# Optimization experiments

Hardware: AMD Instinct MI355X
Metric: run time of the kernel (lower is better)

## Reference

```python
import jax, jax.numpy as jnp
import numpy as np

B, S, H = 2, 2048, 2048
NH, NKV, HD = 16, 4, 128
THETA = 10000.0


def _rope_cos_sin(seq_len, head_dim, theta, dtype):
    inv_freq = 1.0 / (theta ** (jnp.arange(0, head_dim, 2, dtype=jnp.float32) / head_dim))
    t = jnp.arange(seq_len, dtype=jnp.float32)
    freqs = t[:, None] * inv_freq[None, :]          # [S, HD/2]
    emb = jnp.concatenate([freqs, freqs], axis=-1)  # [S, HD]
    return jnp.cos(emb).astype(dtype), jnp.sin(emb).astype(dtype)


def _rotate_half(x):
    d = x.shape[-1] // 2
    return jnp.concatenate([-x[..., d:], x[..., :d]], axis=-1)


def setup_inputs() -> dict:
    key = jax.random.key(0)
    ks = jax.random.split(key, 5)
    x = jax.random.normal(ks[0], (B, S, H), dtype=jnp.float32)
    Wq = jax.random.normal(ks[1], (NH * HD, H), dtype=jnp.float32) * 0.02
    Wk = jax.random.normal(ks[2], (NKV * HD, H), dtype=jnp.float32) * 0.02
    Wv = jax.random.normal(ks[3], (NKV * HD, H), dtype=jnp.float32) * 0.02
    Wo = jax.random.normal(ks[4], (H, H), dtype=jnp.float32) * 0.02
    causal = jnp.tril(jnp.ones((S, S), dtype=bool))
    attention_mask = jnp.where(causal, 0.0, -1e9).astype(jnp.float32)[None, None]  # [1,1,S,S]
    return {"x": x, "attention_mask": attention_mask, "Wq": Wq, "Wk": Wk, "Wv": Wv, "Wo": Wo}


def reference(x, attention_mask, Wq, Wk, Wv, Wo):
    b, s, _ = x.shape
    q = (x @ Wq.T).reshape(b, s, NH, HD).transpose(0, 2, 1, 3)    # [b,nh,s,hd]
    k = (x @ Wk.T).reshape(b, s, NKV, HD).transpose(0, 2, 1, 3)   # [b,nkv,s,hd]
    v = (x @ Wv.T).reshape(b, s, NKV, HD).transpose(0, 2, 1, 3)
    cos, sin = _rope_cos_sin(s, HD, THETA, x.dtype)               # [s,hd] each
    cos = cos[None, None]; sin = sin[None, None]
    q = q * cos + _rotate_half(q) * sin
    k = k * cos + _rotate_half(k) * sin
    rep = NH // NKV
    k = jnp.repeat(k, rep, axis=1)                                 # [b,nh,s,hd]
    v = jnp.repeat(v, rep, axis=1)
    scores = jnp.einsum('bhqd,bhkd->bhqk', q, k) / jnp.sqrt(jnp.asarray(HD, x.dtype))
    scores = scores + attention_mask
    attn = jax.nn.softmax(scores, axis=-1)
    out = jnp.einsum('bhqk,bhkd->bhqd', attn, v)                   # [b,nh,s,hd]
    out = out.transpose(0, 2, 1, 3).reshape(b, s, NH * HD)
    return out @ Wo.T
```

## Files before the change

kernel.cpp:

```cpp
#include <hip/hip_runtime.h>

typedef unsigned short u16;
typedef __bf16 bf16x8 __attribute__((ext_vector_type(8)));
typedef float f32x4 __attribute__((ext_vector_type(4)));
typedef short s16x4 __attribute__((ext_vector_type(4)));

#define S_LEN  2048
#define NHEADS 16
#define NKVH   4
#define HDIM   128
#define BB     2
#define MROWS  4096
#define QKV_N  3072
#define HID    2048

__device__ __forceinline__ u16 f2b(float f) {
  union { float f; unsigned u; } x; x.f = f;
  unsigned r = x.u + 0x7fffu + ((x.u >> 16) & 1u);
  return (u16)(r >> 16);
}
__device__ __forceinline__ float b2f(u16 v) {
  union { unsigned u; float f; } x; x.u = ((unsigned)v) << 16;
  return x.f;
}
__device__ __forceinline__ void gload_lds16(const u16* g, u16* l) {
  __builtin_amdgcn_global_load_lds((__attribute__((address_space(1))) void*)g,
                                   (__attribute__((address_space(3))) void*)l,
                                   16, 0, 0);
}
__device__ __forceinline__ unsigned cvtpk(float lo, float hi) {
  unsigned r;
  asm("v_cvt_pk_bf16_f32 %0, %1, %2" : "=v"(r) : "v"(lo), "v"(hi));
  return r;
}
#if __has_builtin(__builtin_amdgcn_mfma_f32_16x16x16bf16_1k)
__device__ __forceinline__ f32x4 mfma16(s16x4 a, s16x4 b, f32x4 c) {
  return __builtin_amdgcn_mfma_f32_16x16x16bf16_1k(a, b, c, 0, 0, 0);
}
#else
__device__ __forceinline__ f32x4 mfma16(s16x4 a, s16x4 b, f32x4 c) {
  f32x4 d;
  asm volatile("v_mfma_f32_16x16x16_bf16 %0, %1, %2, %3"
               : "=v"(d) : "v"(a), "v"(b), "v"(c));
  return d;
}
#endif

#define PB_X   8192
#define PB_WQ  (PB_X + 4096)
#define PB_WK  (PB_WQ + 1024)
#define PB_WV  (PB_WK + 1024)
#define PB_WO  (PB_WV + 4096)
#define PB_CS  (PB_WO + 512)
__global__ void k_prep(const float* __restrict__ x,
                       const float* __restrict__ Wq, const float* __restrict__ Wk,
                       const float* __restrict__ Wv, const float* __restrict__ Wo,
                       u16* __restrict__ xb, u16* __restrict__ Wqkvb,
                       u16* __restrict__ Wob, float* __restrict__ cs)
{
  const int bid = blockIdx.x, tid = threadIdx.x;
  const float* src; u16* dst; int i;
  if (bid < PB_X)       { i = bid * 256 + tid;            src = x;  dst = xb; }
  else if (bid < PB_WQ) { i = (bid - PB_X) * 256 + tid;   src = Wq; dst = Wqkvb; }
  else if (bid < PB_WK) { i = (bid - PB_WQ) * 256 + tid;  src = Wk; dst = Wqkvb + (size_t)2048 * HID; }
  else if (bid < PB_WV) { i = (bid - PB_WK) * 256 + tid;  src = Wv; dst = Wqkvb + (size_t)2560 * HID; }
  else if (bid < PB_WO) { i = (bid - PB_WV) * 256 + tid;  src = Wo; dst = Wob; }
  else {
    const int p = (bid - PB_WO) * 256 + tid;
    const int s = p >> 6, j = p & 63;
    float inv = expf(-(float)j * 0.14391156831212787f);
    float ang = (float)s * inv;
    float c, sn; sincosf(ang, &sn, &c);
    cs[p * 2 + 0] = c; cs[p * 2 + 1] = sn;
    return;
  }
  float4 v = ((const float4*)src)[i];
  ushort4 o;
  o.x = f2b(v.x); o.y = f2b(v.y); o.z = f2b(v.z); o.w = f2b(v.w);
  ((ushort4*)dst)[i] = o;
}

template <int OUT_BF16>
__global__ __launch_bounds__(256) void k_gemm_bt(
    const u16* __restrict__ A, const u16* __restrict__ Bm, void* __restrict__ Cv,
    int M, int N, int K)
{
  __shared__ u16 Al[128 * 32];
  __shared__ u16 Bl[128 * 32];
  const int tid = threadIdx.x;
  const int wave = tid >> 6, lane = tid & 63;
  const int l15 = lane & 15, l4 = lane >> 4;
  const int wr = wave >> 1, wc = wave & 1;
  const int row0 = blockIdx.y * 128, col0 = blockIdx.x * 128;

  f32x4 zero = {0.f, 0.f, 0.f, 0.f};
  f32x4 acc[4][4];
#pragma unroll
  for (int m = 0; m < 4; ++m)
#pragma unroll
    for (int n = 0; n < 4; ++n) acc[m][n] = zero;

  const int e0 = lane * 8;
  for (int kb = 0; kb < K; kb += 32) {
#pragma unroll
    for (int it = 0; it < 2; ++it) {
      const int chunk = it * 4 + wave;
      const int e = chunk * 512 + e0;
      const int r = e >> 5, c = e & 31;
      gload_lds16(A + (size_t)(row0 + r) * K + kb + c, Al + chunk * 512);
      gload_lds16(Bm + (size_t)(col0 + r) * K + kb + c, Bl + chunk * 512);
    }
    __syncthreads();
    bf16x8 af[4], bfv[4];
#pragma unroll
    for (int m = 0; m < 4; ++m)
      af[m] = *(const bf16x8*)(Al + (wr * 64 + m * 16 + l15) * 32 + l4 * 8);
#pragma unroll
    for (int n = 0; n < 4; ++n)
      bfv[n] = *(const bf16x8*)(Bl + (wc * 64 + n * 16 + l15) * 32 + l4 * 8);
#pragma unroll
    for (int m = 0; m < 4; ++m)
#pragma unroll
      for (int n = 0; n < 4; ++n)
        acc[m][n] = __builtin_amdgcn_mfma_f32_16x16x32_bf16(af[m], bfv[n], acc[m][n], 0, 0, 0);
    __syncthreads();
  }
#pragma unroll
  for (int m = 0; m < 4; ++m) {
    const int r = row0 + wr * 64 + m * 16 + l4 * 4;
#pragma unroll
    for (int n = 0; n < 4; ++n) {
      const int c = col0 + wc * 64 + n * 16 + l15;
#pragma unroll
      for (int j = 0; j < 4; ++j) {
        const float v = acc[m][n][j];
        if (OUT_BF16) ((u16*)Cv)[(size_t)(r + j) * N + c] = f2b(v);
        else          ((float*)Cv)[(size_t)(r + j) * N + c] = v;
      }
    }
  }
}

__global__ __launch_bounds__(256) void k_ropev(
    const u16* __restrict__ qkv, const float* __restrict__ cs,
    u16* __restrict__ Qr, u16* __restrict__ Kr, u16* __restrict__ Vt)
{
  const int blk = blockIdx.x;
  const int b = blk >> 8, s0 = (blk & 255) << 3;
  const int tid = threadIdx.x;
  const float S2 = 0.08838834764831845f * 1.4426950408889634f;
#pragma unroll
  for (int p = tid; p < 8192; p += 256) {
    const int s = p >> 10, rem = p & 1023, h = rem >> 6, j = rem & 63;
    const int sg = s0 + s;
    const float c = cs[(sg * 64 + j) * 2], sn = cs[(sg * 64 + j) * 2 + 1];
    const u16* src = qkv + (size_t)(b * S_LEN + sg) * QKV_N + h * 128;
    const float x0 = b2f(src[j]), x1 = b2f(src[64 + j]);
    const size_t base = ((size_t)(b * NHEADS + h) * S_LEN + sg) * HDIM;
    Qr[base + j]      = f2b((x0 * c - x1 * sn) * S2);
    Qr[base + 64 + j] = f2b((x1 * c + x0 * sn) * S2);
  }
#pragma unroll
  for (int p = tid; p < 2048; p += 256) {
    const int s = p >> 8, rem = p & 255, h = rem >> 6, j = rem & 63;
    const int sg = s0 + s;
    const float c = cs[(sg * 64 + j) * 2], sn = cs[(sg * 64 + j) * 2 + 1];
    const u16* src = qkv + (size_t)(b * S_LEN + sg) * QKV_N + 2048 + h * 128;
    const float x0 = b2f(src[j]), x1 = b2f(src[64 + j]);
    const size_t base = ((size_t)(b * NKVH + h) * S_LEN + sg) * HDIM;
    Kr[base + j]      = f2b(x0 * c - x1 * sn);
    Kr[base + 64 + j] = f2b(x1 * c + x0 * sn);
  }
#pragma unroll
  for (int vi = 0; vi < 2; ++vi) {
    const int idx = vi * 256 + tid, h = idx >> 7, d = idx & 127;
    union { u16 u[8]; uint4 v; } bb;
#pragma unroll
    for (int s = 0; s < 8; ++s)
      bb.u[s] = qkv[(size_t)(b * S_LEN + s0 + s) * QKV_N + 2560 + idx];
    *(uint4*)(Vt + ((size_t)(b * NKVH + h) * HDIM + d) * S_LEN + s0) = bb.v;
  }
}

__device__ __forceinline__ void attn_qtile(
    int qt, int lastPhase,
    const u16* __restrict__ Q, const u16* __restrict__ Kg, const u16* __restrict__ Vg,
    u16* __restrict__ Out, int bh,
    u16* Kl0, u16* Kl1, u16* Vl0, u16* Vl1,
    const int (&ko)[4], const int (&vo)[4],
    int wave, int lane, int& cur)
{
  const int l15 = lane & 15, l4 = lane >> 4;
  const int b = bh >> 4, h = bh & 15;
  const int qw0 = qt * 64 + wave * 16;
  const u16* Qg = Q + ((size_t)bh * S_LEN + qw0) * HDIM;

  bf16x8 qf[4];
#pragma unroll
  for (int kc = 0; kc < 4; ++kc)
    qf[kc] = *(const bf16x8*)(Qg + l15 * HDIM + kc * 32 + l4 * 8);

  f32x4 zero = {0.f, 0.f, 0.f, 0.f};
  f32x4 oacc[8];
#pragma unroll
  for (int i = 0; i < 8; ++i) oacc[i] = zero;
  float m_r = -1e30f, l_p = 0.f;

  const int nt = qt + 1;
  const int qg = qw0 + l15;

  for (int t = 0; t < nt; ++t) {
    const int kt = t * 64;
    u16* Vb = cur ? Vl1 : Vl0;
#pragma unroll
    for (int it = 0; it < 4; ++it)
      gload_lds16(Vg + (size_t)vo[it] + kt, Vb + (it * 4 + wave) * 512);
    const int hasNext = (t + 1 < nt) || (!lastPhase);
    const int ktn = (t + 1 < nt) ? kt + 64 : 0;
    u16* Kn = cur ? Kl0 : Kl1;
    if (hasNext) {
#pragma unroll
      for (int it = 0; it < 4; ++it)
        gload_lds16(Kg + (size_t)ktn * HDIM + ko[it], Kn + (it * 4 + wave) * 512);
      asm volatile("s_waitcnt vmcnt(8)" ::: "memory");
    } else {
      asm volatile("s_waitcnt vmcnt(4)" ::: "memory");
    }
    __builtin_amdgcn_sched_barrier(0);
    __builtin_amdgcn_s_barrier();
    __builtin_amdgcn_sched_barrier(0);

    const char* Kb = (const char*)(cur ? Kl1 : Kl0);
    f32x4 s[4];
#pragma unroll
    for (int n = 0; n < 4; ++n) s[n] = zero;
    __builtin_amdgcn_s_setprio(1);
#pragma unroll
    for (int n = 0; n < 4; ++n) {
      const int row = n * 16 + l15;
#pragma unroll
      for (int kc = 0; kc < 4; ++kc) {
        const int ab = (row * 256 + kc * 64 + l4 * 16) ^ ((row & 7) << 4);
        bf16x8 kf = *(const bf16x8*)(Kb + ab);
        s[n] = __builtin_amdgcn_mfma_f32_16x16x32_bf16(kf, qf[kc], s[n], 0, 0, 0);
      }
    }
    __builtin_amdgcn_s_setprio(0);
    float sv[4][4];
    if (kt + 63 > qw0) {
#pragma unroll
      for (int n = 0; n < 4; ++n)
#pragma unroll
        for (int j = 0; j < 4; ++j) {
          float x = s[n][j];
          if (kt + n * 16 + l4 * 4 + j > qg) x = -1e30f;
          sv[n][j] = x;
        }
    } else {
#pragma unroll
      for (int n = 0; n < 4; ++n)
#pragma unroll
        for (int j = 0; j < 4; ++j) sv[n][j] = s[n][j];
    }
    float pm = sv[0][0];
#pragma unroll
    for (int n = 0; n < 4; ++n)
#pragma unroll
      for (int j = 0; j < 4; ++j) pm = fmaxf(pm, sv[n][j]);
    if (!__all(pm <= m_r + 11.5416f)) {
      float pf = fmaxf(pm, __shfl_xor(pm, 16, 64));
      pf = fmaxf(pf, __shfl_xor(pf, 32, 64));
      const float mn = fmaxf(m_r, pf);
      const float sc = exp2f(m_r - mn);
      m_r = mn;
      l_p *= sc;
      float scq[4];
#pragma unroll
      for (int j = 0; j < 4; ++j) scq[j] = __shfl(sc, l4 * 4 + j, 64);
#pragma unroll
      for (int nd = 0; nd < 8; ++nd)
#pragma unroll
        for (int j = 0; j < 4; ++j) oacc[nd][j] *= scq[j];
    }
    union { unsigned u[2]; s16x4 v; } a[4];
#pragma unroll
    for (int n = 0; n < 4; ++n) {
      const float p0 = exp2f(sv[n][0] - m_r);
      const float p1 = exp2f(sv[n][1] - m_r);
      const float p2 = exp2f(sv[n][2] - m_r);
      const float p3 = exp2f(sv[n][3] - m_r);
      l_p += (p0 + p1) + (p2 + p3);
      a[n].u[0] = cvtpk(p0, p1);
      a[n].u[1] = cvtpk(p2, p3);
    }
    if (hasNext) asm volatile("s_waitcnt vmcnt(4)" ::: "memory");
    else         asm volatile("s_waitcnt vmcnt(0)" ::: "memory");
    __builtin_amdgcn_sched_barrier(0);
    __builtin_amdgcn_s_barrier();
    __builtin_amdgcn_sched_barrier(0);
    __builtin_amdgcn_s_setprio(1);
#pragma unroll
    for (int nd = 0; nd < 8; ++nd) {
      const int d = nd * 16 + l15;
      const int rowb = d * 128, swz = (d & 7) << 4;
#pragma unroll
      for (int n = 0; n < 4; ++n) {
        const int ab = (rowb + n * 32 + l4 * 8) ^ swz;
        s16x4 vf = *(const s16x4*)((const char*)Vb + ab);
        oacc[nd] = mfma16(a[n].v, vf, oacc[nd]);
      }
    }
    __builtin_amdgcn_s_setprio(0);
    cur ^= 1;
  }

  l_p += __shfl_xor(l_p, 16, 64);
  l_p += __shfl_xor(l_p, 32, 64);
  float il[4];
#pragma unroll
  for (int j = 0; j < 4; ++j) il[j] = 1.f / __shfl(l_p, l4 * 4 + j, 64);
  const size_t obase = ((size_t)b * S_LEN + qw0 + l4 * 4) * HID + h * HDIM;
#pragma unroll
  for (int nd = 0; nd < 8; ++nd)
#pragma unroll
    for (int j = 0; j < 4; ++j)
      Out[obase + (size_t)j * HID + nd * 16 + l15] = f2b(oacc[nd][j] * il[j]);
}

__global__ __launch_bounds__(256) void k_attn(
    const u16* __restrict__ Q, const u16* __restrict__ Kr,
    const u16* __restrict__ Vt, u16* __restrict__ Out)
{
  __shared__ u16 Kl[2][64 * 128];
  __shared__ u16 Vl[2][128 * 64];
  const int tid = threadIdx.x;
  const int wave = tid >> 6, lane = tid & 63;
  const int bh = blockIdx.x;
  const int pairi = blockIdx.y;
  const int b = bh >> 4, h = bh & 15;
  const int kvh = h >> 2;

  const u16* Kg = Kr + (size_t)(b * NKVH + kvh) * S_LEN * HDIM;
  const u16* Vg = Vt + (size_t)(b * NKVH + kvh) * HDIM * S_LEN;

  int ko[4], vo[4];
#pragma unroll
  for (int it = 0; it < 4; ++it) {
    const int c = it * 4 + wave;
    const int L = c * 1024 + lane * 16;
    const int r = L >> 8;  const int w2 = (L & 255) ^ ((r & 7) << 4);
    ko[it] = r * HDIM + (w2 >> 1);
    const int d = L >> 7;  const int wv = (L & 127) ^ ((d & 7) << 4);
    vo[it] = d * S_LEN + (wv >> 1);
  }
#pragma unroll
  for (int it = 0; it < 4; ++it)
    gload_lds16(Kg + ko[it], &Kl[0][(it * 4 + wave) * 512]);

  int cur = 0;
  attn_qtile(31 - pairi, 0, Q, Kg, Vg, Out, bh, &Kl[0][0], &Kl[1][0],
             &Vl[0][0], &Vl[1][0], ko, vo, wave, lane, cur);
  attn_qtile(pairi,      1, Q, Kg, Vg, Out, bh, &Kl[0][0], &Kl[1][0],
             &Vl[0][0], &Vl[1][0], ko, vo, wave, lane, cur);
}

extern "C" void kernel_launch(void* const* d_in, const int* in_sizes, int n_in,
                              void* d_out, int out_size, void* d_ws, size_t ws_size,
                              hipStream_t stream)
{
  const float* x  = (const float*)d_in[0];
  const float* Wq = (const float*)d_in[2];
  const float* Wk = (const float*)d_in[3];
  const float* Wv = (const float*)d_in[4];
  const float* Wo = (const float*)d_in[5];
  float* out = (float*)d_out;

  u16* xb    = (u16*)d_ws;
  u16* Wqkvb = xb    + (size_t)MROWS * HID;
  u16* Wob   = Wqkvb + (size_t)QKV_N * HID;
  u16* qkv   = Wob   + (size_t)HID * HID;
  u16* Qr    = qkv   + (size_t)MROWS * QKV_N;
  u16* Kr    = Qr    + (size_t)BB * NHEADS * S_LEN * HDIM;
  u16* Vt    = Kr    + (size_t)BB * NKVH * S_LEN * HDIM;
  u16* attn  = Vt    + (size_t)BB * NKVH * S_LEN * HDIM;
  float* cs  = (float*)(attn + (size_t)MROWS * HID);

  k_prep<<<dim3(PB_CS), 256, 0, stream>>>(x, Wq, Wk, Wv, Wo, xb, Wqkvb, Wob, cs);
  k_gemm_bt<1><<<dim3(QKV_N / 128, MROWS / 128), 256, 0, stream>>>(xb, Wqkvb, qkv, MROWS, QKV_N, HID);
  k_ropev<<<dim3(BB * 256), 256, 0, stream>>>(qkv, cs, Qr, Kr, Vt);
  k_attn<<<dim3(BB * NHEADS, 16), 256, 0, stream>>>(Qr, Kr, Vt, attn);
  k_gemm_bt<0><<<dim3(HID / 128, MROWS / 128), 256, 0, stream>>>(attn, Wob, out, MROWS, HID, HID);
}
```

Measured before the change: 231.5 us.

## Add 256x256 tiled 8-wave GEMM with staggered prefetch for QKV projection

Adds a new GEMM kernel for the QKV projection that computes a 256x256 output tile with 512 threads. It uses double-buffered, swizzled LDS loaded by direct global-to-LDS copies, issues the A and B prefetches in stages between four MFMA groups, and remaps block IDs in an XCD-aware order. The larger tile raises arithmetic intensity per LDS and global load and overlaps memory with compute. In exchange it uses 64 KB of LDS and many more registers per thread, and the grid shrinks to 192 blocks, which may leave some compute units underused.

```diff
diff --git a/kernel.cpp b/kernel.cpp
--- a/kernel.cpp
+++ b/kernel.cpp
@@ -45,6 +45,10 @@
   return d;
 }
 #endif
+
+#define SBAR() do { __builtin_amdgcn_sched_barrier(0); \
+                    __builtin_amdgcn_s_barrier();      \
+                    __builtin_amdgcn_sched_barrier(0); } while (0)
 
 #define PB_X   8192
 #define PB_WQ  (PB_X + 4096)
@@ -80,6 +84,135 @@
   ((ushort4*)dst)[i] = o;
 }
 
+#define MFMA_GRP(AV, BV, MO, NO)                                              \
+  __builtin_amdgcn_s_setprio(1);                                              \
+  _Pragma("unroll") for (int kk = 0; kk < 2; ++kk)                            \
+  _Pragma("unroll") for (int mm = 0; mm < 4; ++mm)                            \
+  _Pragma("unroll") for (int nn = 0; nn < 2; ++nn)                            \
+    acc[(MO) + mm][(NO) + nn] = __builtin_amdgcn_mfma_f32_16x16x32_bf16(      \
+        AV[kk][mm], BV[kk][nn], acc[(MO) + mm][(NO) + nn], 0, 0, 0);          \
+  __builtin_amdgcn_s_setprio(0);
+
+template <int OUT_BF16>
+__global__ __launch_bounds__(512, 2) void k_gemm256(
+    const u16* __restrict__ A, const u16* __restrict__ Bm, void* __restrict__ Cv,
+    int M, int N, int K)
+{
+  __shared__ u16 AL[2][2][8192];
+  __shared__ u16 BL[2][2][8192];
+  const int tid = threadIdx.x;
+  const int wave = tid >> 6, lane = tid & 63;
+  const int l15 = lane & 15, l4 = lane >> 4;
+  const int wr = wave >> 2, wc = wave & 3;
+  const int gx = gridDim.x;
+  const int nwg = gx * gridDim.y;
+  int bid = blockIdx.y * gx + blockIdx.x;
+  bid = (bid & 7) * (nwg >> 3) + (bid >> 3);
+  const int col0 = (bid % gx) * 256, row0 = (bid / gx) * 256;
+
+  int srcOff[2], dstD[2];
+#pragma unroll
+  for (int li = 0; li < 2; ++li) {
+    const int D = (li * 512 + tid) * 16;
+    const int off_p = D & 1023, si = D >> 10;
+    const int off_l = off_p ^ (((off_p >> 9) & 1) << 5);
+    const int R = si >> 1, C = si & 1;
+    const int row = R * 16 + (off_l >> 6);
+    const int colb = C * 64 + (off_l & 63);
+    srcOff[li] = row * K + (colb >> 1);
+    dstD[li] = D;
+  }
+  const int laneoff = (l15 * 64 + l4 * 16) ^ ((l15 >> 3) << 5);
+
+  auto stage = [&](const u16* __restrict__ G, int grow0, int kb, u16* lds) {
+#pragma unroll
+    for (int li = 0; li < 2; ++li)
+      gload_lds16(G + (size_t)grow0 * K + kb + srcOff[li],
+                  (u16*)((char*)lds + dstD[li]));
+  };
+
+  f32x4 acc[8][4];
+#pragma unroll
+  for (int m = 0; m < 8; ++m)
+#pragma unroll
+    for (int n = 0; n < 4; ++n) acc[m][n] = f32x4{0.f, 0.f, 0.f, 0.f};
+
+  const int nk = K >> 6;
+  stage(A,  row0,       0,  &AL[0][0][0]);
+  stage(A,  row0 + 128, 0,  &AL[0][1][0]);
+  stage(Bm, col0,       0,  &BL[0][0][0]);
+  stage(Bm, col0 + 128, 0,  &BL[0][1][0]);
+  stage(A,  row0,       64, &AL[1][0][0]);
+  stage(A,  row0 + 128, 64, &AL[1][1][0]);
+  asm volatile("s_waitcnt vmcnt(4)" ::: "memory");
+  SBAR();
+
+  for (int t = 0; t < nk; ++t) {
+    const int bi = t & 1;
+    const bool sB = (t + 1 < nk);
+    const bool sA = (t + 2 < nk);
+    const char* Ab = (const char*)&AL[bi][wr][0];
+    const char* Bb = (const char*)&BL[bi][wc >> 1][0] + (wc & 1) * 8192;
+    bf16x8 a0[2][4], a1[2][4], b0[2][2], b1[2][2];
+#pragma unroll
+    for (int kk = 0; kk < 2; ++kk)
+#pragma unroll
+      for (int m = 0; m < 4; ++m)
+        a0[kk][m] = *(const bf16x8*)(Ab + m * 2048 + kk * 1024 + laneoff);
+#pragma unroll
+    for (int kk = 0; kk < 2; ++kk)
+#pragma unroll
+      for (int n = 0; n < 2; ++n)
+        b0[kk][n] = *(const bf16x8*)(Bb + n * 2048 + kk * 1024 + laneoff);
+    if (sB) stage(Bm, col0, (t + 1) * 64, &BL[bi ^ 1][0][0]);
+    SBAR();
+    MFMA_GRP(a0, b0, 0, 0);
+    SBAR();
+#pragma unroll
+    for (int kk = 0; kk < 2; ++kk)
+#pragma unroll
+      for (int m = 0; m < 4; ++m)
+        a1[kk][m] = *(const bf16x8*)(Ab + (m + 4) * 2048 + kk * 1024 + laneoff);
+    if (sB) stage(Bm, col0 + 128, (t + 1) * 64, &BL[bi ^ 1][1][0]);
+    SBAR();
+    MFMA_GRP(a1, b0, 4, 0);
+    SBAR();
+#pragma unroll
+    for (int kk = 0; kk < 2; ++kk)
+#pragma unroll
+      for (int n = 0; n < 2; ++n)
+        b1[kk][n] = *(const bf16x8*)(Bb + (n + 2) * 2048 + kk * 1024 + laneoff);
+    if (sA) stage(A, row0, (t + 2) * 64, &AL[bi][0][0]);
+    SBAR();
+    MFMA_GRP(a1, b1, 4, 2);
+    SBAR();
+    if (sA) {
+      stage(A, row0 + 128, (t + 2) * 64, &AL[bi][1][0]);
+      asm volatile("s_waitcnt vmcnt(4)" ::: "memory");
+    } else if (sB) {
+      asm volatile("s_waitcnt vmcnt(0)" ::: "memory");
+    }
+    SBAR();
+    MFMA_GRP(a0, b1, 0, 2);
+    SBAR();
+  }
+
+#pragma unroll
+  for (int m = 0; m < 8; ++m) {
+    const int r = row0 + wr * 128 + m * 16 + l4 * 4;
+#pragma unroll
+    for (int n = 0; n < 4; ++n) {
+      const int c = col0 + wc * 64 + n * 16 + l15;
+#pragma unroll
+      for (int j = 0; j < 4; ++j) {
+        const float v = acc[m][n][j];
+        if (OUT_BF16) ((u16*)Cv)[(size_t)(r + j) * N + c] = f2b(v);
+        else          ((float*)Cv)[(size_t)(r + j) * N + c] = v;
+      }
+    }
+  }
+}
+
 template <int OUT_BF16>
 __global__ __launch_bounds__(256) void k_gemm_bt(
     const u16* __restrict__ A, const u16* __restrict__ Bm, void* __restrict__ Cv,
@@ -226,9 +359,7 @@
     } else {
       asm volatile("s_waitcnt vmcnt(4)" ::: "memory");
     }
-    __builtin_amdgcn_sched_barrier(0);
-    __builtin_amdgcn_s_barrier();
-    __builtin_amdgcn_sched_barrier(0);
+    SBAR();
 
     const char* Kb = (const char*)(cur ? Kl1 : Kl0);
     f32x4 s[4];
@@ -295,9 +426,7 @@
     }
     if (hasNext) asm volatile("s_waitcnt vmcnt(4)" ::: "memory");
     else         asm volatile("s_waitcnt vmcnt(0)" ::: "memory");
-    __builtin_amdgcn_sched_barrier(0);
-    __builtin_amdgcn_s_barrier();
-    __builtin_amdgcn_sched_barrier(0);
+    SBAR();
     __builtin_amdgcn_s_setprio(1);
 #pragma unroll
     for (int nd = 0; nd < 8; ++nd) {
@@ -386,7 +515,7 @@
   float* cs  = (float*)(attn + (size_t)MROWS * HID);
 
   k_prep<<<dim3(PB_CS), 256, 0, stream>>>(x, Wq, Wk, Wv, Wo, xb, Wqkvb, Wob, cs);
-  k_gemm_bt<1><<<dim3(QKV_N / 128, MROWS / 128), 256, 0, stream>>>(xb, Wqkvb, qkv, MROWS, QKV_N, HID);
+  k_gemm256<1><<<dim3(QKV_N / 256, MROWS / 256), 512, 0, stream>>>(xb, Wqkvb, qkv, MROWS, QKV_N, HID);
   k_ropev<<<dim3(BB * 256), 256, 0, stream>>>(qkv, cs, Qr, Kr, Vt);
   k_attn<<<dim3(BB * NHEADS, 16), 256, 0, stream>>>(Qr, Kr, Vt, attn);
   k_gemm_bt<0><<<dim3(HID / 128, MROWS / 128), 256, 0, stream>>>(attn, Wob, out, MROWS, HID, HID);
```

After: 222.7 us. -3.8%, faster.
